# Optimization experiments

Measured on AMD Instinct MI355X. Metric: run time of the kernel, lower is better.

The kernel has to match this reference:

```python
import jax, jax.numpy as jnp
import numpy as np

DIM, M, K = 768, 48, 256
MK = M * K            # 12288
H = MK // 2           # 6144
MID = int(0.75 * MK)  # 9216
B = 2048
MIN_DIST_FACTOR = 10.0
LN_EPS = 1e-5


def setup_inputs() -> dict:
    key = jax.random.key(0)
    ks = jax.random.split(key, 18)
    s = 0.02  # keep exp(sigma_logits) tame
    return {
        "x": jax.random.normal(ks[0], (B, DIM), jnp.float32),
        "codebook": jax.random.normal(ks[1], (M, K, DIM // M), jnp.float32),
        "rot1": jnp.eye(DIM) + s * jax.random.normal(ks[2], (DIM, DIM), jnp.float32),
        "ln_g": jnp.ones((DIM,), jnp.float32),
        "ln_b": jnp.zeros((DIM,), jnp.float32),
        "l1_w": s * jax.random.normal(ks[3], (MID, DIM), jnp.float32),
        "l1_b": jnp.zeros((MID,), jnp.float32),
        "mu_w": s * jax.random.normal(ks[4], (H, MID), jnp.float32),
        "mu_b": jnp.zeros((H,), jnp.float32),
        "sig_w": s * jax.random.normal(ks[5], (H, MID), jnp.float32),
        "sig_b": jnp.zeros((H,), jnp.float32),
        "rot2": jnp.eye(H) + s * jax.random.normal(ks[6], (H, H), jnp.float32),
        "l2_w": s * jax.random.normal(ks[7], (MK, H), jnp.float32),
        "l2_b": jnp.zeros((MK,), jnp.float32),
        "interp_param": jax.random.normal(ks[8], (1,), jnp.float32),
        "vae_noise": jax.random.normal(ks[9], (B, H), jnp.float32),
        "gumbel_noise": -jnp.log(-jnp.log(
            jax.random.uniform(ks[10], (B, M, K), jnp.float32, 1e-10, 1.0))),
    }


def _layernorm(x, g, b):
    mu = jnp.mean(x, axis=-1, keepdims=True)
    var = jnp.mean((x - mu) ** 2, axis=-1, keepdims=True)
    return (x - mu) * jax.lax.rsqrt(var + LN_EPS) * g + b


def reference(x, codebook, rot1, ln_g, ln_b, l1_w, l1_b, mu_w, mu_b,
              sig_w, sig_b, rot2, l2_w, l2_b, interp_param,
              vae_noise, gumbel_noise):
    x_rot = x @ rot1.T                                   # [B, DIM]
    xn = _layernorm(x_rot, ln_g, ln_b)
    h1 = jax.nn.relu(xn @ l1_w.T + l1_b)                 # [B, MID]
    mu = h1 @ mu_w.T + mu_b                              # [B, H]
    sigma = jnp.exp(h1 @ sig_w.T + sig_b)                # [B, H]
    z = mu + sigma * vae_noise                           # reparameterized sample
    h = jnp.tanh(z)
    h_rot = h @ rot2.T                                   # [B, H]
    a = jax.nn.relu(h_rot @ l2_w.T + l2_b)               # [B, MK]
    a_r = a.reshape(-1, M, K)                            # [B, M, K]
    # PQ distances: [B, M, 1, d] vs [1, M, K, d] -> [B, M, K]
    d = DIM // M
    xs = x_rot.reshape(-1, M, 1, d)
    cs = codebook.reshape(1, M, K, d)
    dist = jnp.sum((cs - xs) ** 2, axis=-1)
    min_dist = jax.nn.one_hot(jnp.argmin(dist, axis=-1), K, dtype=jnp.float32)
    interp = jax.nn.sigmoid(interp_param[0])
    logits = (1.0 - interp) * a_r + interp * MIN_DIST_FACTOR * min_dist
    # hard gumbel-softmax, tau=1
    y_soft = jax.nn.softmax(logits + gumbel_noise, axis=-1)
    y_hard = jax.nn.one_hot(jnp.argmax(y_soft, axis=-1), K, dtype=y_soft.dtype)
    s = y_hard - jax.lax.stop_gradient(y_soft) + y_soft
    return s
```

## Files before the change

kernel.cpp:

```cpp
#include <hip/hip_runtime.h>
#include <cstddef>
#include <cstdint>

constexpr int kDIM = 768;
constexpr int kM   = 48;
constexpr int kK   = 256;
constexpr int kB   = 2048;
constexpr int kMID = 9216;
constexpr int kH   = 6144;
constexpr int kMK  = 12288;

using bf8v  = __attribute__((ext_vector_type(8))) short;
using f32x4 = __attribute__((ext_vector_type(4))) float;
using s8v   = __attribute__((ext_vector_type(8))) short;

#define GLL16(SRC, DST) __builtin_amdgcn_global_load_lds( \
    (const __attribute__((address_space(1))) void*)(SRC), \
    (__attribute__((address_space(3))) void*)(DST), 16, 0, 0)

template<bool HASBIAS, int EPI, typename OUT_T>
__global__ __launch_bounds__(256)
void gemm_nt_acc64(const float* __restrict__ A, const float* __restrict__ W,
                   const float* __restrict__ bias, OUT_T* C,
                   const float* zslog, const float* __restrict__ znoise,
                   int N, int Kd)
{
  __shared__ float As[16][132];
  __shared__ float Bs[16][132];
  const int tid  = (int)threadIdx.x;
  const int row0 = (int)blockIdx.y * 128;
  const int col0 = (int)blockIdx.x * 128;
  const int ty = tid >> 4, tx = tid & 15;
  const int i0 = ty * 8, j0 = tx * 8;
  const int fi1 = tid >> 2;
  const int fi2 = fi1 + 64;
  const int kc  = (tid & 3) * 4;

  const float* Ap1 = A + (size_t)(row0 + fi1) * Kd + kc;
  const float* Ap2 = A + (size_t)(row0 + fi2) * Kd + kc;
  const float* Wp1 = W + (size_t)(col0 + fi1) * Kd + kc;
  const float* Wp2 = W + (size_t)(col0 + fi2) * Kd + kc;

  double acc[8][8];
#pragma unroll
  for (int r = 0; r < 8; ++r)
#pragma unroll
    for (int c = 0; c < 8; ++c) acc[r][c] = 0.0;

  for (int kt = 0; kt < Kd; kt += 16) {
    const float4 a1 = *(const float4*)(Ap1 + kt);
    const float4 a2 = *(const float4*)(Ap2 + kt);
    const float4 b1 = *(const float4*)(Wp1 + kt);
    const float4 b2 = *(const float4*)(Wp2 + kt);
    As[kc + 0][fi1] = a1.x; As[kc + 1][fi1] = a1.y; As[kc + 2][fi1] = a1.z; As[kc + 3][fi1] = a1.w;
    As[kc + 0][fi2] = a2.x; As[kc + 1][fi2] = a2.y; As[kc + 2][fi2] = a2.z; As[kc + 3][fi2] = a2.w;
    Bs[kc + 0][fi1] = b1.x; Bs[kc + 1][fi1] = b1.y; Bs[kc + 2][fi1] = b1.z; Bs[kc + 3][fi1] = b1.w;
    Bs[kc + 0][fi2] = b2.x; Bs[kc + 1][fi2] = b2.y; Bs[kc + 2][fi2] = b2.z; Bs[kc + 3][fi2] = b2.w;
    __syncthreads();
#pragma unroll
    for (int kk = 0; kk < 16; ++kk) {
      const float4 av0 = *(const float4*)&As[kk][i0];
      const float4 av1 = *(const float4*)&As[kk][i0 + 4];
      const float4 bv0 = *(const float4*)&Bs[kk][j0];
      const float4 bv1 = *(const float4*)&Bs[kk][j0 + 4];
      const float ar[8] = {av0.x, av0.y, av0.z, av0.w, av1.x, av1.y, av1.z, av1.w};
      const float br[8] = {bv0.x, bv0.y, bv0.z, bv0.w, bv1.x, bv1.y, bv1.z, bv1.w};
      double bd[8];
#pragma unroll
      for (int c = 0; c < 8; ++c) bd[c] = (double)br[c];
#pragma unroll
      for (int r = 0; r < 8; ++r) {
        const double ad = (double)ar[r];
#pragma unroll
        for (int c = 0; c < 8; ++c)
          acc[r][c] = fma(ad, bd[c], acc[r][c]);
      }
    }
    __syncthreads();
  }

  double bvv[8];
#pragma unroll
  for (int c = 0; c < 8; ++c) bvv[c] = 0.0;
  if (HASBIAS) {
#pragma unroll
    for (int c = 0; c < 8; ++c) bvv[c] = (double)bias[col0 + j0 + c];
  }

#pragma unroll
  for (int r = 0; r < 8; ++r) {
    const size_t gbase = (size_t)(row0 + i0 + r) * N + col0 + j0;
    double o[8];
#pragma unroll
    for (int c = 0; c < 8; ++c) {
      double v = acc[r][c];
      if (HASBIAS) v += bvv[c];
      if (EPI == 1) v = fmax(v, 0.0);
      if (EPI == 2) {
        const double sg = exp((double)zslog[gbase + c]);
        v = tanh(v + sg * (double)znoise[gbase + c]);
      }
      o[c] = v;
    }
    if constexpr (sizeof(OUT_T) == 4) {
      float* dst = (float*)C + gbase;
      ((float4*)dst)[0] = make_float4((float)o[0], (float)o[1], (float)o[2], (float)o[3]);
      ((float4*)dst)[1] = make_float4((float)o[4], (float)o[5], (float)o[6], (float)o[7]);
    } else {
      double* dst = (double*)C + gbase;
#pragma unroll
      for (int c = 0; c < 8; ++c) dst[c] = o[c];
    }
  }
}

__device__ __forceinline__ unsigned short bf16rn(float f) {
  const unsigned u = __float_as_uint(f);
  return (unsigned short)((u + 0x7FFFu + ((u >> 16) & 1u)) >> 16);
}

__global__ __launch_bounds__(256)
void split3_k(const float* __restrict__ in, short* __restrict__ out, size_t n)
{
  const size_t i = ((size_t)blockIdx.x * 256 + threadIdx.x) * 8;
  const float4 v0 = *(const float4*)(in + i);
  const float4 v1 = *(const float4*)(in + i + 4);
  const float f[8] = {v0.x, v0.y, v0.z, v0.w, v1.x, v1.y, v1.z, v1.w};
  s8v o1, o2, o3;
#pragma unroll
  for (int j = 0; j < 8; ++j) {
    const unsigned short b1 = bf16rn(f[j]);
    const float r1 = f[j] - __uint_as_float((unsigned)b1 << 16);
    const unsigned short b2 = bf16rn(r1);
    const float r2 = r1 - __uint_as_float((unsigned)b2 << 16);
    const unsigned short b3 = bf16rn(r2);
    o1[j] = (short)b1; o2[j] = (short)b2; o3[j] = (short)b3;
  }
  *(s8v*)(out + i)         = o1;
  *(s8v*)(out + n + i)     = o2;
  *(s8v*)(out + 2 * n + i) = o3;
}

template<bool HASBIAS, bool RELU>
__global__ __launch_bounds__(256, 2)
void gemm3_bf16(const short* __restrict__ A3, const short* __restrict__ W3,
                const float* __restrict__ bias, float* __restrict__ C,
                int N, int Kd, int nbx)
{
  __shared__ short lds[6][4096];
  short* smem = &lds[0][0];
  const char* smemc = (const char*)smem;

  int wg = (int)blockIdx.x;
  const int nwg = (int)gridDim.x;
  if ((nwg & 7) == 0) { const int q = nwg >> 3; wg = (wg & 7) * q + (wg >> 3); }
  const int nby = kB / 128;
  const int by = wg % nby, bx = wg / nby;
  const int row0 = by * 128, col0 = bx * 128;

  const int tid = (int)threadIdx.x;
  const int l = tid & 63, w = tid >> 6;
  const int wr = (w & 1) * 64, wc = (w >> 1) * 64;

  const size_t planeAB = (size_t)2048 * Kd * 2;
  const size_t planeWB = (size_t)N * Kd * 2;
  const char* A3b = (const char*)A3;
  const char* W3b = (const char*)W3;

  const int su = 2 * w;
  const int r0 = su * 16 + (l >> 2), r1 = r0 + 16;
  const int qsw = (((l & 3) ^ ((l >> 3) & 3)) << 4);
  const size_t offA0 = (size_t)(row0 + r0) * Kd * 2 + qsw;
  const size_t offA1 = (size_t)(row0 + r1) * Kd * 2 + qsw;
  const size_t offW0 = (size_t)(col0 + r0) * Kd * 2 + qsw;
  const size_t offW1 = (size_t)(col0 + r1) * Kd * 2 + qsw;
  short* dA0 = smem + (su + 0) * 512;
  short* dA1 = smem + (su + 1) * 512;

  int aoff[3][4], boff[3][4];
#pragma unroll
  for (int p = 0; p < 3; ++p) {
#pragma unroll
    for (int t = 0; t < 4; ++t) {
      const int Ra = wr + t * 16 + (l & 15);
      aoff[p][t] = p * 8192 + Ra * 64 + ((((l >> 4)) ^ ((Ra >> 1) & 3)) << 4);
      const int Rb = wc + t * 16 + (l & 15);
      boff[p][t] = (3 + p) * 8192 + Rb * 64 + ((((l >> 4)) ^ ((Rb >> 1) & 3)) << 4);
    }
  }

  f32x4 acc[4][4];
#pragma unroll
  for (int i = 0; i < 4; ++i)
#pragma unroll
    for (int j = 0; j < 4; ++j) acc[i][j] = f32x4{0.f, 0.f, 0.f, 0.f};

  for (int kt = 0; kt < Kd; kt += 32) {
    const size_t kb = (size_t)kt * 2;
#pragma unroll
    for (int t = 0; t < 3; ++t) {
      GLL16(A3b + t * planeAB + offA0 + kb, dA0 + t * 4096);
      GLL16(A3b + t * planeAB + offA1 + kb, dA1 + t * 4096);
    }
#pragma unroll
    for (int t = 0; t < 3; ++t) {
      GLL16(W3b + t * planeWB + offW0 + kb, dA0 + (3 + t) * 4096);
      GLL16(W3b + t * planeWB + offW1 + kb, dA1 + (3 + t) * 4096);
    }
    __syncthreads();

    bf8v af[3][4], bf_[3][4];
#pragma unroll
    for (int p = 0; p < 3; ++p)
#pragma unroll
      for (int t = 0; t < 4; ++t) {
        af[p][t]  = *(const bf8v*)(smemc + aoff[p][t]);
        bf_[p][t] = *(const bf8v*)(smemc + boff[p][t]);
      }
#pragma unroll
    for (int tr = 0; tr < 4; ++tr)
#pragma unroll
      for (int tc = 0; tc < 4; ++tc) {
        f32x4 c = acc[tr][tc];
        c = __builtin_amdgcn_mfma_f32_16x16x32_bf16(af[0][tr], bf_[0][tc], c, 0, 0, 0);
        c = __builtin_amdgcn_mfma_f32_16x16x32_bf16(af[0][tr], bf_[1][tc], c, 0, 0, 0);
        c = __builtin_amdgcn_mfma_f32_16x16x32_bf16(af[1][tr], bf_[0][tc], c, 0, 0, 0);
        c = __builtin_amdgcn_mfma_f32_16x16x32_bf16(af[0][tr], bf_[2][tc], c, 0, 0, 0);
        c = __builtin_amdgcn_mfma_f32_16x16x32_bf16(af[2][tr], bf_[0][tc], c, 0, 0, 0);
        c = __builtin_amdgcn_mfma_f32_16x16x32_bf16(af[1][tr], bf_[1][tc], c, 0, 0, 0);
        acc[tr][tc] = c;
      }
    __syncthreads();
  }

#pragma unroll
  for (int tc = 0; tc < 4; ++tc) {
    const int colg = col0 + wc + tc * 16 + (l & 15);
    float bv = 0.f;
    if (HASBIAS) bv = bias[colg];
#pragma unroll
    for (int tr = 0; tr < 4; ++tr) {
      const int rowg0 = row0 + wr + tr * 16 + ((l >> 4) << 2);
#pragma unroll
      for (int g = 0; g < 4; ++g) {
        float v = acc[tr][tc][g];
        if (HASBIAS) v += bv;
        if (RELU)    v = fmaxf(v, 0.f);
        C[(size_t)(rowg0 + g) * N + colg] = v;
      }
    }
  }
}

__global__ __launch_bounds__(256)
void layernorm_k(const double* __restrict__ in, const float* __restrict__ g,
                 const float* __restrict__ b, float* __restrict__ out)
{
  const int row = (int)blockIdx.x;
  const int tid = (int)threadIdx.x;
  const double* x = in + (size_t)row * kDIM;
  const double v0 = x[tid], v1 = x[tid + 256], v2 = x[tid + 512];
  __shared__ double red[8];
  double s = v0 + v1 + v2;
#pragma unroll
  for (int off = 32; off; off >>= 1) s += __shfl_xor(s, off);
  if ((tid & 63) == 0) red[tid >> 6] = s;
  __syncthreads();
  const double mean = (red[0] + red[1] + red[2] + red[3]) * (1.0 / 768.0);
  const double d0 = v0 - mean, d1 = v1 - mean, d2 = v2 - mean;
  double q = d0 * d0 + d1 * d1 + d2 * d2;
#pragma unroll
  for (int off = 32; off; off >>= 1) q += __shfl_xor(q, off);
  if ((tid & 63) == 0) red[4 + (tid >> 6)] = q;
  __syncthreads();
  const double var = (red[4] + red[5] + red[6] + red[7]) * (1.0 / 768.0);
  const double rs = 1.0 / sqrt(var + 1e-5);
  float* y = out + (size_t)row * kDIM;
  y[tid]       = (float)(d0 * rs * (double)g[tid]       + (double)b[tid]);
  y[tid + 256] = (float)(d1 * rs * (double)g[tid + 256] + (double)b[tid + 256]);
  y[tid + 512] = (float)(d2 * rs * (double)g[tid + 512] + (double)b[tid + 512]);
}

__global__ __launch_bounds__(256)
void zh_k(const float* __restrict__ mu, float* slog_h, const float* __restrict__ noise)
{
  const size_t i = (size_t)blockIdx.x * 256 + threadIdx.x;
  const double z = (double)mu[i] + exp((double)slog_h[i]) * (double)noise[i];
  slog_h[i] = (float)tanh(z);
}

__global__ __launch_bounds__(256)
void mindist_k(const double* __restrict__ xrot, const float* __restrict__ cb,
               int* __restrict__ minidx)
{
  const int wid  = (int)blockIdx.x * 4 + ((int)threadIdx.x >> 6);
  const int lane = (int)threadIdx.x & 63;
  const int bi = wid / kM, mi = wid % kM;
  const double* xv = xrot + (size_t)bi * kDIM + mi * 16;
  double xs[16];
#pragma unroll
  for (int d = 0; d < 16; ++d) xs[d] = xv[d];
  const float* cm = cb + (size_t)mi * (kK * 16);
  double best = 1e300; int bidx = 0;
#pragma unroll
  for (int j = 0; j < 4; ++j) {
    const int k = lane * 4 + j;
    const float* ck = cm + k * 16;
    double s = 0.0;
#pragma unroll
    for (int d = 0; d < 16; ++d) {
      const double t = (double)ck[d] - xs[d];
      s = fma(t, t, s);
    }
    if (s < best) { best = s; bidx = k; }
  }
#pragma unroll
  for (int off = 32; off; off >>= 1) {
    const double ob = __shfl_xor(best, off);
    const int    oi = __shfl_xor(bidx, off);
    if (ob < best || (ob == best && oi < bidx)) { best = ob; bidx = oi; }
  }
  if (lane == 0) minidx[wid] = bidx;
}

__global__ __launch_bounds__(256)
void finalize_k(float* a, const float* __restrict__ gumbel,
                const int* __restrict__ minidx, const float* __restrict__ interp_param)
{
  const int wid  = (int)blockIdx.x * 4 + ((int)threadIdx.x >> 6);
  const int lane = (int)threadIdx.x & 63;
  const double interp = 1.0 / (1.0 + exp(-(double)interp_param[0]));
  const double w = 1.0 - interp;
  const double bonus = interp * 10.0;
  const int mi = minidx[wid];
  const size_t base = (size_t)wid * 256 + lane * 4;
  const float4 av = *(const float4*)&a[base];
  const float4 gv = *(const float4*)&gumbel[base];
  const int k0 = lane * 4;
  double lg[4] = {w * (double)av.x + (double)gv.x,
                  w * (double)av.y + (double)gv.y,
                  w * (double)av.z + (double)gv.z,
                  w * (double)av.w + (double)gv.w};
#pragma unroll
  for (int j = 0; j < 4; ++j)
    if (k0 + j == mi) lg[j] += bonus;

  double best = -1e300; int bk = 0;
#pragma unroll
  for (int j = 0; j < 4; ++j)
    if (lg[j] > best) { best = lg[j]; bk = k0 + j; }
#pragma unroll
  for (int off = 32; off; off >>= 1) {
    const double ob = __shfl_xor(best, off);
    const int    oi = __shfl_xor(bk, off);
    if (ob > best || (ob == best && oi < bk)) { best = ob; bk = oi; }
  }
  float4 o;
  o.x = (k0 + 0 == bk) ? 1.f : 0.f;
  o.y = (k0 + 1 == bk) ? 1.f : 0.f;
  o.z = (k0 + 2 == bk) ? 1.f : 0.f;
  o.w = (k0 + 3 == bk) ? 1.f : 0.f;
  *(float4*)&a[base] = o;
}

extern "C" void kernel_launch(void* const* d_in, const int* in_sizes, int n_in,
                              void* d_out, int out_size, void* d_ws, size_t ws_size,
                              hipStream_t stream)
{
  const float* x      = (const float*)d_in[0];
  const float* cb     = (const float*)d_in[1];
  const float* rot1   = (const float*)d_in[2];
  const float* ln_g   = (const float*)d_in[3];
  const float* ln_b   = (const float*)d_in[4];
  const float* l1_w   = (const float*)d_in[5];
  const float* l1_b   = (const float*)d_in[6];
  const float* mu_w   = (const float*)d_in[7];
  const float* mu_b   = (const float*)d_in[8];
  const float* sig_w  = (const float*)d_in[9];
  const float* sig_b  = (const float*)d_in[10];
  const float* rot2   = (const float*)d_in[11];
  const float* l2_w   = (const float*)d_in[12];
  const float* l2_b   = (const float*)d_in[13];
  const float* interp = (const float*)d_in[14];
  const float* noise  = (const float*)d_in[15];
  const float* gumb   = (const float*)d_in[16];

  const dim3 blk(256);
  float* aout = (float*)d_out;

  const size_t nXrot = (size_t)kB * kDIM;
  const size_t nH1   = (size_t)kB * kMID;
  const size_t nHH   = (size_t)kB * kH;
  const size_t NEED  = nXrot * 8 + nXrot * 4 + nH1 * 4 + nHH * 4 + nHH * 4
                     + nH1 * 3 * 2 + (size_t)kMK * kH * 3 * 2 + (size_t)kB * kM * 4;

  if (ws_size >= NEED) {
    char* p = (char*)d_ws;
    double* x_rotd = (double*)p;              p += nXrot * 8;
    float*  xn     = (float*)p;               p += nXrot * 4;
    float*  h1     = (float*)p;               p += nH1 * 4;
    float*  mu     = (float*)p;               p += nHH * 4;
    float*  slog   = (float*)p;               p += nHH * 4;
    short*  As3    = (short*)p;               p += nH1 * 3 * 2;
    short*  Ws3    = (short*)p;               p += (size_t)kMK * kH * 3 * 2;
    int*    midx   = (int*)p;

    gemm_nt_acc64<false, 0, double><<<dim3(kDIM / 128, kB / 128), blk, 0, stream>>>(
        x, rot1, nullptr, x_rotd, nullptr, nullptr, kDIM, kDIM);
    layernorm_k<<<dim3(kB), blk, 0, stream>>>(x_rotd, ln_g, ln_b, xn);
    mindist_k<<<dim3(kB * kM / 4), blk, 0, stream>>>(x_rotd, cb, midx);

    split3_k<<<dim3((unsigned)(nXrot / 2048)), blk, 0, stream>>>(xn, As3, nXrot);
    split3_k<<<dim3((unsigned)((size_t)kMID * kDIM / 2048)), blk, 0, stream>>>(l1_w, Ws3, (size_t)kMID * kDIM);
    gemm3_bf16<true, true><<<dim3(kMID / 128 * (kB / 128)), blk, 0, stream>>>(
        As3, Ws3, l1_b, h1, kMID, kDIM, kMID / 128);

    split3_k<<<dim3((unsigned)(nH1 / 2048)), blk, 0, stream>>>(h1, As3, nH1);
    split3_k<<<dim3((unsigned)((size_t)kH * kMID / 2048)), blk, 0, stream>>>(mu_w, Ws3, (size_t)kH * kMID);
    gemm3_bf16<true, false><<<dim3(kH / 128 * (kB / 128)), blk, 0, stream>>>(
        As3, Ws3, mu_b, mu, kH, kMID, kH / 128);
    split3_k<<<dim3((unsigned)((size_t)kH * kMID / 2048)), blk, 0, stream>>>(sig_w, Ws3, (size_t)kH * kMID);
    gemm3_bf16<true, false><<<dim3(kH / 128 * (kB / 128)), blk, 0, stream>>>(
        As3, Ws3, sig_b, slog, kH, kMID, kH / 128);

    zh_k<<<dim3((unsigned)(nHH / 256)), blk, 0, stream>>>(mu, slog, noise);

    split3_k<<<dim3((unsigned)(nHH / 2048)), blk, 0, stream>>>(slog, As3, nHH);
    split3_k<<<dim3((unsigned)((size_t)kH * kH / 2048)), blk, 0, stream>>>(rot2, Ws3, (size_t)kH * kH);
    gemm3_bf16<false, false><<<dim3(kH / 128 * (kB / 128)), blk, 0, stream>>>(
        As3, Ws3, nullptr, h1, kH, kH, kH / 128);

    split3_k<<<dim3((unsigned)(nHH / 2048)), blk, 0, stream>>>(h1, As3, nHH);
    split3_k<<<dim3((unsigned)((size_t)kMK * kH / 2048)), blk, 0, stream>>>(l2_w, Ws3, (size_t)kMK * kH);
    gemm3_bf16<true, true><<<dim3(kMK / 128 * (kB / 128)), blk, 0, stream>>>(
        As3, Ws3, l2_b, aout, kMK, kH, kMK / 128);

    finalize_k<<<dim3(kB * kM / 4), blk, 0, stream>>>(aout, gumb, midx, interp);
    return;
  }

  char* wsb    = (char*)d_ws;
  double* x_rotd = (double*)wsb;
  float*  xn     = (float*)(wsb + (size_t)kB * kDIM * 8);
  float*  h1     = xn   + (size_t)kB * kDIM;
  float*  slog   = h1   + (size_t)kB * kMID;
  int*    midx   = (int*)(slog + (size_t)kB * kH);
  float*  hrot   = h1;

  gemm_nt_acc64<false, 0, double><<<dim3(kDIM / 128, kB / 128), blk, 0, stream>>>(
      x, rot1, nullptr, x_rotd, nullptr, nullptr, kDIM, kDIM);
  layernorm_k<<<dim3(kB), blk, 0, stream>>>(x_rotd, ln_g, ln_b, xn);
  mindist_k<<<dim3(kB * kM / 4), blk, 0, stream>>>(x_rotd, cb, midx);
  gemm_nt_acc64<true, 1, float><<<dim3(kMID / 128, kB / 128), blk, 0, stream>>>(
      xn, l1_w, l1_b, h1, nullptr, nullptr, kMID, kDIM);
  gemm_nt_acc64<true, 0, float><<<dim3(kH / 128, kB / 128), blk, 0, stream>>>(
      h1, sig_w, sig_b, slog, nullptr, nullptr, kH, kMID);
  gemm_nt_acc64<true, 2, float><<<dim3(kH / 128, kB / 128), blk, 0, stream>>>(
      h1, mu_w, mu_b, slog, slog, noise, kH, kMID);
  gemm_nt_acc64<false, 0, float><<<dim3(kH / 128, kB / 128), blk, 0, stream>>>(
      slog, rot2, nullptr, hrot, nullptr, nullptr, kH, kH);
  gemm_nt_acc64<true, 1, float><<<dim3(kMK / 128, kB / 128), blk, 0, stream>>>(
      hrot, l2_w, l2_b, aout, nullptr, nullptr, kMK, kH);
  finalize_k<<<dim3(kB * kM / 4), blk, 0, stream>>>(aout, gumb, midx, interp);
}
```

Measured before the change: 6.301 ms.

## Switch bf16x3 GEMM to 32x32 MFMA with double-buffered weight tiles

The split-bf16 GEMM moves from 16x16x32 MFMA tiles to 32x32x16 MFMA tiles, which cuts the number of LDS fragment reads per MFMA. The weight tile is now double-buffered in LDS, so the next K-step's weights load while the current step computes. The A tile is reloaded after a barrier. LDS use grows to 72KB per block, which may limit occupancy under the 2-block launch bound, and the output write pattern changes to match the 32x32 accumulator layout.

```diff
diff --git a/kernel.cpp b/kernel.cpp
--- a/kernel.cpp
+++ b/kernel.cpp
@@ -10,9 +10,10 @@
 constexpr int kH   = 6144;
 constexpr int kMK  = 12288;
 
-using bf8v  = __attribute__((ext_vector_type(8))) short;
-using f32x4 = __attribute__((ext_vector_type(4))) float;
-using s8v   = __attribute__((ext_vector_type(8))) short;
+using bf8v   = __attribute__((ext_vector_type(8))) short;
+using f32x4  = __attribute__((ext_vector_type(4))) float;
+using f32x16 = __attribute__((ext_vector_type(16))) float;
+using s8v    = __attribute__((ext_vector_type(8))) short;
 
 #define GLL16(SRC, DST) __builtin_amdgcn_global_load_lds( \
     (const __attribute__((address_space(1))) void*)(SRC), \
@@ -147,9 +148,7 @@
                 const float* __restrict__ bias, float* __restrict__ C,
                 int N, int Kd, int nbx)
 {
-  __shared__ short lds[6][4096];
-  short* smem = &lds[0][0];
-  const char* smemc = (const char*)smem;
+  __shared__ char lds[73728];
 
   int wg = (int)blockIdx.x;
   const int nwg = (int)gridDim.x;
@@ -174,79 +173,115 @@
   const size_t offA1 = (size_t)(row0 + r1) * Kd * 2 + qsw;
   const size_t offW0 = (size_t)(col0 + r0) * Kd * 2 + qsw;
   const size_t offW1 = (size_t)(col0 + r1) * Kd * 2 + qsw;
-  short* dA0 = smem + (su + 0) * 512;
-  short* dA1 = smem + (su + 1) * 512;
-
-  int aoff[3][4], boff[3][4];
+  const int c0 = su * 1024, c1 = c0 + 1024;
+
+  int aoff[3][2][2], boff[3][2][2];
 #pragma unroll
   for (int p = 0; p < 3; ++p) {
 #pragma unroll
-    for (int t = 0; t < 4; ++t) {
-      const int Ra = wr + t * 16 + (l & 15);
-      aoff[p][t] = p * 8192 + Ra * 64 + ((((l >> 4)) ^ ((Ra >> 1) & 3)) << 4);
-      const int Rb = wc + t * 16 + (l & 15);
-      boff[p][t] = (3 + p) * 8192 + Rb * 64 + ((((l >> 4)) ^ ((Rb >> 1) & 3)) << 4);
-    }
-  }
-
-  f32x4 acc[4][4];
-#pragma unroll
-  for (int i = 0; i < 4; ++i)
-#pragma unroll
-    for (int j = 0; j < 4; ++j) acc[i][j] = f32x4{0.f, 0.f, 0.f, 0.f};
-
-  for (int kt = 0; kt < Kd; kt += 32) {
-    const size_t kb = (size_t)kt * 2;
+    for (int t = 0; t < 2; ++t) {
+#pragma unroll
+      for (int kh = 0; kh < 2; ++kh) {
+        const int Ra = wr + t * 32 + (l & 31);
+        aoff[p][t][kh] = p * 8192 + Ra * 64 +
+                         (((kh * 2 + (l >> 5)) ^ ((Ra >> 1) & 3)) << 4);
+        const int Rb = wc + t * 32 + (l & 31);
+        boff[p][t][kh] = p * 8192 + Rb * 64 +
+                         (((kh * 2 + (l >> 5)) ^ ((Rb >> 1) & 3)) << 4);
+      }
+    }
+  }
+
+  f32x16 acc[2][2];
+#pragma unroll
+  for (int i = 0; i < 2; ++i)
+#pragma unroll
+    for (int j = 0; j < 2; ++j)
+#pragma unroll
+      for (int g = 0; g < 16; ++g) acc[i][j][g] = 0.f;
+
+  const int NITER = Kd >> 5;
+
+  {
+    char* wb = lds + 24576;
 #pragma unroll
     for (int t = 0; t < 3; ++t) {
-      GLL16(A3b + t * planeAB + offA0 + kb, dA0 + t * 4096);
-      GLL16(A3b + t * planeAB + offA1 + kb, dA1 + t * 4096);
-    }
-#pragma unroll
-    for (int t = 0; t < 3; ++t) {
-      GLL16(W3b + t * planeWB + offW0 + kb, dA0 + (3 + t) * 4096);
-      GLL16(W3b + t * planeWB + offW1 + kb, dA1 + (3 + t) * 4096);
-    }
+      GLL16(A3b + t * planeAB + offA0, lds + t * 8192 + c0);
+      GLL16(A3b + t * planeAB + offA1, lds + t * 8192 + c1);
+      GLL16(W3b + t * planeWB + offW0, wb + t * 8192 + c0);
+      GLL16(W3b + t * planeWB + offW1, wb + t * 8192 + c1);
+    }
+  }
+  __syncthreads();
+
+  for (int it = 0; it < NITER; ++it) {
+    const int par = it & 1;
+    const char* wbase = lds + 24576 + par * 24576;
+
+    if (it + 1 < NITER) {
+      const size_t kb = (size_t)(it + 1) * 64;
+      char* wb = lds + 24576 + (par ^ 1) * 24576;
+#pragma unroll
+      for (int t = 0; t < 3; ++t) {
+        GLL16(W3b + t * planeWB + offW0 + kb, wb + t * 8192 + c0);
+        GLL16(W3b + t * planeWB + offW1 + kb, wb + t * 8192 + c1);
+      }
+    }
+
+    bf8v af[3][2][2], bf_[3][2][2];
+#pragma unroll
+    for (int p = 0; p < 3; ++p)
+#pragma unroll
+      for (int t = 0; t < 2; ++t)
+#pragma unroll
+        for (int kh = 0; kh < 2; ++kh) {
+          af[p][t][kh]  = *(const bf8v*)(lds + aoff[p][t][kh]);
+          bf_[p][t][kh] = *(const bf8v*)(wbase + boff[p][t][kh]);
+        }
+#pragma unroll
+    for (int kh = 0; kh < 2; ++kh)
+#pragma unroll
+      for (int tr = 0; tr < 2; ++tr)
+#pragma unroll
+        for (int tc = 0; tc < 2; ++tc) {
+          f32x16 c = acc[tr][tc];
+          c = __builtin_amdgcn_mfma_f32_32x32x16_bf16(af[0][tr][kh], bf_[0][tc][kh], c, 0, 0, 0);
+          c = __builtin_amdgcn_mfma_f32_32x32x16_bf16(af[0][tr][kh], bf_[1][tc][kh], c, 0, 0, 0);
+          c = __builtin_amdgcn_mfma_f32_32x32x16_bf16(af[1][tr][kh], bf_[0][tc][kh], c, 0, 0, 0);
+          c = __builtin_amdgcn_mfma_f32_32x32x16_bf16(af[0][tr][kh], bf_[2][tc][kh], c, 0, 0, 0);
+          c = __builtin_amdgcn_mfma_f32_32x32x16_bf16(af[2][tr][kh], bf_[0][tc][kh], c, 0, 0, 0);
+          c = __builtin_amdgcn_mfma_f32_32x32x16_bf16(af[1][tr][kh], bf_[1][tc][kh], c, 0, 0, 0);
+          acc[tr][tc] = c;
+        }
+
     __syncthreads();
 
-    bf8v af[3][4], bf_[3][4];
-#pragma unroll
-    for (int p = 0; p < 3; ++p)
-#pragma unroll
-      for (int t = 0; t < 4; ++t) {
-        af[p][t]  = *(const bf8v*)(smemc + aoff[p][t]);
-        bf_[p][t] = *(const bf8v*)(smemc + boff[p][t]);
+    if (it + 1 < NITER) {
+      const size_t kb = (size_t)(it + 1) * 64;
+#pragma unroll
+      for (int t = 0; t < 3; ++t) {
+        GLL16(A3b + t * planeAB + offA0 + kb, lds + t * 8192 + c0);
+        GLL16(A3b + t * planeAB + offA1 + kb, lds + t * 8192 + c1);
       }
-#pragma unroll
-    for (int tr = 0; tr < 4; ++tr)
-#pragma unroll
-      for (int tc = 0; tc < 4; ++tc) {
-        f32x4 c = acc[tr][tc];
-        c = __builtin_amdgcn_mfma_f32_16x16x32_bf16(af[0][tr], bf_[0][tc], c, 0, 0, 0);
-        c = __builtin_amdgcn_mfma_f32_16x16x32_bf16(af[0][tr], bf_[1][tc], c, 0, 0, 0);
-        c = __builtin_amdgcn_mfma_f32_16x16x32_bf16(af[1][tr], bf_[0][tc], c, 0, 0, 0);
-        c = __builtin_amdgcn_mfma_f32_16x16x32_bf16(af[0][tr], bf_[2][tc], c, 0, 0, 0);
-        c = __builtin_amdgcn_mfma_f32_16x16x32_bf16(af[2][tr], bf_[0][tc], c, 0, 0, 0);
-        c = __builtin_amdgcn_mfma_f32_16x16x32_bf16(af[1][tr], bf_[1][tc], c, 0, 0, 0);
-        acc[tr][tc] = c;
-      }
+    }
     __syncthreads();
   }
 
 #pragma unroll
-  for (int tc = 0; tc < 4; ++tc) {
-    const int colg = col0 + wc + tc * 16 + (l & 15);
+  for (int tc = 0; tc < 2; ++tc) {
+    const int colg = col0 + wc + tc * 32 + (l & 31);
     float bv = 0.f;
     if (HASBIAS) bv = bias[colg];
 #pragma unroll
-    for (int tr = 0; tr < 4; ++tr) {
-      const int rowg0 = row0 + wr + tr * 16 + ((l >> 4) << 2);
-#pragma unroll
-      for (int g = 0; g < 4; ++g) {
-        float v = acc[tr][tc][g];
+    for (int tr = 0; tr < 2; ++tr) {
+      const int rbase = row0 + wr + tr * 32 + ((l >> 5) << 2);
+#pragma unroll
+      for (int r = 0; r < 16; ++r) {
+        const int rowg = rbase + (r & 3) + 8 * (r >> 2);
+        float v = acc[tr][tc][r];
         if (HASBIAS) v += bv;
         if (RELU)    v = fmaxf(v, 0.f);
-        C[(size_t)(rowg0 + g) * N + colg] = v;
+        C[(size_t)rowg * N + colg] = v;
       }
     }
   }
```

Measured after the change: 6.570 ms. +4.3%, slower.
